# Performance work log

Hardware: AMD Instinct MI355X
Metric: run time of the kernel (lower is better)

## Reference

```python
import jax, jax.numpy as jnp
import numpy as np

B, C, H, W = 4, 64, 64, 64
DQ = 64            # query/key dim (hardcoded 64 in the module)
FP_DIM = 128       # fingerprint_dim
SCALE = 1.0 / 8.0  # 1/sqrt(64)


def setup_inputs() -> dict:
    key = jax.random.key(0)
    ks = jax.random.split(key, 12)
    s = 0.05
    return {
        "x": jax.random.normal(ks[0], (B, C, H, W), jnp.float32),
        "fingerprint": jax.random.normal(ks[1], (B, FP_DIM), jnp.float32),
        # 1x1 conv weights stored as [out_ch, in_ch]
        "Wq": jax.random.normal(ks[2], (DQ, C), jnp.float32) * s,
        "bq": jax.random.normal(ks[3], (DQ,), jnp.float32) * s,
        "Wk": jax.random.normal(ks[4], (DQ, C), jnp.float32) * s,
        "bk": jax.random.normal(ks[5], (DQ,), jnp.float32) * s,
        "Wv": jax.random.normal(ks[6], (C, C), jnp.float32) * s,
        "bv": jax.random.normal(ks[7], (C,), jnp.float32) * s,
        "Wo": jax.random.normal(ks[8], (C, C), jnp.float32) * s,
        "bo": jax.random.normal(ks[9], (C,), jnp.float32) * s,
        "Wfp": jax.random.normal(ks[10], (DQ, FP_DIM), jnp.float32) * s,
        "bfp": jax.random.normal(ks[11], (DQ,), jnp.float32) * s,
    }


def reference(x, fingerprint, Wq, bq, Wk, bk, Wv, bv, Wo, bo, Wfp, bfp):
    b, c, h, w = x.shape
    # fingerprint projection: Linear(fingerprint_dim, 64)
    fp_proj = fingerprint @ Wfp.T + bfp                      # [B, 64]
    # 1x1 convs as channel einsums
    q = jnp.einsum('bchw,oc->bohw', x, Wq) + bq[None, :, None, None]  # [B,64,H,W]
    k = jnp.einsum('bchw,oc->bohw', x, Wk) + bk[None, :, None, None]  # [B,64,H,W]
    v = jnp.einsum('bchw,oc->bohw', x, Wv) + bv[None, :, None, None]  # [B,C,H,W]
    qf = q.reshape(b, DQ, h * w)   # [B,64,N]
    kf = k.reshape(b, DQ, h * w)   # [B,64,N]
    vf = v.reshape(b, c, h * w)    # [B,C,N]
    # attn[b,i,j] = <q_i, k_j>/sqrt(64), softmax over keys j
    attn = jax.nn.softmax(jnp.einsum('bdi,bdj->bij', qf, kf) * SCALE, axis=2)  # [B,N,N]
    out = jnp.einsum('bcj,bij->bci', vf, attn).reshape(b, c, h, w)
    # fingerprint-gated modulation map
    attn_map = jax.nn.sigmoid(jnp.einsum('bdhw,bd->bhw', q, fp_proj))[:, None]  # [B,1,H,W]
    out = out * attn_map + x
    out = jnp.einsum('bchw,oc->bohw', out, Wo) + bo[None, :, None, None]
    return out
```

## Files before the change

### kernel.cpp

```cpp
#include <hip/hip_runtime.h>
#include <cstdint>
#include <cstddef>

#define B_    4
#define C_    64
#define N_    4096
#define FPD_  128
#define QSCALE_ (0.125f * 1.4426950408889634f)

typedef short bf16x8 __attribute__((ext_vector_type(8)));
typedef float f32x4  __attribute__((ext_vector_type(4)));

__device__ inline unsigned short f2bf(float f) {
    union { float f; unsigned int u; } v; v.f = f;
    unsigned int u = v.u;
    return (unsigned short)((u + 0x7FFFu + ((u >> 16) & 1u)) >> 16);
}

__global__ __launch_bounds__(256) void prep_kernel(
    const float* __restrict__ fp, const float* __restrict__ Wfp,
    const float* __restrict__ bfp,
    const float* __restrict__ Wq, const float* __restrict__ bq,
    const float* __restrict__ Wk, const float* __restrict__ bk,
    const float* __restrict__ Wv, const float* __restrict__ bv,
    const float* __restrict__ Wo,
    float* __restrict__ fp_proj, unsigned short* __restrict__ Wb,
    float* __restrict__ bs)
{
    int tid = threadIdx.x;
    if (blockIdx.x == 0) {
        int b = tid >> 6, d = tid & 63;
        float acc = bfp[d];
        for (int i = 0; i < FPD_; ++i)
            acc = fmaf(fp[b * FPD_ + i], Wfp[d * FPD_ + i], acc);
        fp_proj[b * 64 + d] = acc;
        if (tid < 64) {
            bs[tid]       = bq[tid] * QSCALE_;
            bs[64 + tid]  = bk[tid];
            bs[128 + tid] = bv[tid];
        }
    } else {
        int g = (blockIdx.x - 1) * 256 + tid;
        int which = g >> 12, l = g & 4095;
        float v;
        if (which == 0)      v = Wq[l] * QSCALE_;
        else if (which == 1) v = Wk[l];
        else if (which == 2) v = Wv[l];
        else                 v = Wo[l];
        Wb[g] = f2bf(v);
    }
}

__global__ __launch_bounds__(256) void qkv_kernel(
    const float* __restrict__ x, const unsigned short* __restrict__ Wb,
    const float* __restrict__ bs, const float* __restrict__ fp_proj,
    float* __restrict__ gate,
    unsigned short* __restrict__ Qb, unsigned short* __restrict__ Kb,
    unsigned short* __restrict__ Vb)
{
    __shared__ unsigned short xT[64 * 72];
    __shared__ unsigned short rp[64 * 72];

    int tid = threadIdx.x;
    int b  = blockIdx.x >> 6;
    int p0 = (blockIdx.x & 63) << 6;
    const float* xb = x + (size_t)b * (C_ * N_) + p0;

    for (int i = 0; i < 16; ++i) {
        int l = tid + i * 256;
        int c = l >> 6, p = l & 63;
        xT[p * 72 + c] = f2bf(xb[(size_t)c * N_ + p]);
    }
    __syncthreads();

    int lane = tid & 63;
    int wv   = __builtin_amdgcn_readfirstlane(tid >> 6);
    int quad = lane >> 4, l16 = lane & 15;
    int prow = wv * 16 + l16;

    bf16x8 bx0 = *reinterpret_cast<bf16x8*>(&xT[prow * 72 + quad * 8]);
    bf16x8 bx1 = *reinterpret_cast<bf16x8*>(&xT[prow * 72 + 32 + quad * 8]);

    float gp = 0.f;

    for (int pass = 0; pass < 3; ++pass) {
        #pragma unroll
        for (int t4 = 0; t4 < 4; ++t4) {
            int ot = pass * 4 + t4;
            const unsigned short* Wg = Wb + ot * 1024;
            bf16x8 a0 = *reinterpret_cast<const bf16x8*>(&Wg[l16 * 64 + quad * 8]);
            bf16x8 a1 = *reinterpret_cast<const bf16x8*>(&Wg[l16 * 64 + 32 + quad * 8]);
            f32x4 c4 = (f32x4){0.f, 0.f, 0.f, 0.f};
            c4 = __builtin_amdgcn_mfma_f32_16x16x32_bf16(a0, bx0, c4, 0, 0, 0);
            c4 = __builtin_amdgcn_mfma_f32_16x16x32_bf16(a1, bx1, c4, 0, 0, 0);
            float4 bias = *reinterpret_cast<const float4*>(&bs[ot * 16 + quad * 4]);
            c4[0] += bias.x; c4[1] += bias.y; c4[2] += bias.z; c4[3] += bias.w;
            if (pass == 0) {
                float4 fpp = *reinterpret_cast<const float4*>(
                                 &fp_proj[b * 64 + t4 * 16 + quad * 4]);
                gp = fmaf(c4[0], fpp.x, gp); gp = fmaf(c4[1], fpp.y, gp);
                gp = fmaf(c4[2], fpp.z, gp); gp = fmaf(c4[3], fpp.w, gp);
            }
            if (pass < 2) {
                int dd = t4 * 16 + quad * 4;
                ushort2 u01, u23;
                u01.x = f2bf(c4[0]); u01.y = f2bf(c4[1]);
                u23.x = f2bf(c4[2]); u23.y = f2bf(c4[3]);
                *reinterpret_cast<ushort2*>(&rp[prow * 72 + dd])     = u01;
                *reinterpret_cast<ushort2*>(&rp[prow * 72 + dd + 2]) = u23;
            } else {
                #pragma unroll
                for (int j = 0; j < 4; ++j)
                    rp[(t4 * 16 + quad * 4 + j) * 72 + prow] = f2bf(c4[j]);
            }
        }
        if (pass == 0) {
            gp += __shfl_xor(gp, 16);
            gp += __shfl_xor(gp, 32);
            if (l16 == 0 && quad == 0) {  }
            if (lane < 16) {
                int pos = p0 + wv * 16 + lane;
                float s = gp * (1.0f / QSCALE_);
                gate[b * N_ + pos] = 1.f / (1.f + __expf(-s));
            }
        }
        __syncthreads();
        int row = tid >> 2;
        int cb  = (tid & 3) << 4;
        ushort4 u[4];
        #pragma unroll
        for (int k = 0; k < 4; ++k)
            u[k] = *reinterpret_cast<ushort4*>(&rp[row * 72 + cb + k * 4]);
        if (pass == 0) {
            unsigned short* dst = Qb + ((size_t)b * N_ + p0 + row) * 64 + cb;
            #pragma unroll
            for (int k = 0; k < 4; ++k)
                *reinterpret_cast<ushort4*>(dst + k * 4) = u[k];
        } else if (pass == 1) {
            unsigned short* dst = Kb + ((size_t)b * N_ + p0 + row) * 64 + cb;
            #pragma unroll
            for (int k = 0; k < 4; ++k)
                *reinterpret_cast<ushort4*>(dst + k * 4) = u[k];
        } else {
            unsigned short* dst = Vb + ((size_t)b * 64 + row) * N_ + p0 + cb;
            #pragma unroll
            for (int k = 0; k < 4; ++k)
                *reinterpret_cast<ushort4*>(dst + k * 4) = u[k];
        }
        __syncthreads();
    }
}

__global__ __launch_bounds__(256, 4) void attn_kernel(
    const unsigned short* __restrict__ Qb, const unsigned short* __restrict__ Kb,
    const unsigned short* __restrict__ Vb, float* __restrict__ Oattn,
    float* __restrict__ lsum)
{
    __shared__ unsigned short Ks[64 * 72];
    __shared__ unsigned short Vs[64 * 72];
    __shared__ unsigned short Ps[64 * 72];

    int tid = threadIdx.x;
    int bx  = blockIdx.x;
    int qt  = bx >> 4;
    int grp = bx & 15;
    int b   = grp >> 2;
    int ks  = grp & 3;
    int q0  = qt << 6;
    int kbase = ks << 10;

    int lane = tid & 63;
    int wv   = __builtin_amdgcn_readfirstlane(tid >> 6);
    int quad = lane >> 4, l16 = lane & 15;
    int qs0  = wv << 4;

    const unsigned short* Qg = Qb + ((size_t)b * N_ + q0) * 64;
    bf16x8 aq0 = *reinterpret_cast<const bf16x8*>(&Qg[(qs0 + l16) * 64 + quad * 8]);
    bf16x8 aq1 = *reinterpret_cast<const bf16x8*>(&Qg[(qs0 + l16) * 64 + 32 + quad * 8]);

    const unsigned short* Kg = Kb + ((size_t)b * N_ + kbase) * 64;
    const unsigned short* Vg = Vb + (size_t)b * 64 * N_ + kbase;

    int r0 = tid >> 4;
    int cc = (tid & 15) << 2;

    ushort4 kr[4], vr[4];
    #pragma unroll
    for (int i = 0; i < 4; ++i) {
        int r = r0 + 16 * i;
        kr[i] = *reinterpret_cast<const ushort4*>(&Kg[(size_t)r * 64 + cc]);
        vr[i] = *reinterpret_cast<const ushort4*>(&Vg[(size_t)r * N_ + cc]);
    }

    f32x4 oacc[4]; f32x4 lacc = (f32x4){0.f, 0.f, 0.f, 0.f};
    #pragma unroll
    for (int cs = 0; cs < 4; ++cs) oacc[cs] = (f32x4){0.f, 0.f, 0.f, 0.f};
    bf16x8 ones;
    #pragma unroll
    for (int i = 0; i < 8; ++i) ones[i] = (short)0x3F80;

    for (int kt = 0; kt < 16; ++kt) {
        __syncthreads();
        #pragma unroll
        for (int i = 0; i < 4; ++i) {
            int r = r0 + 16 * i;
            *reinterpret_cast<ushort4*>(&Ks[r * 72 + cc]) = kr[i];
            *reinterpret_cast<ushort4*>(&Vs[r * 72 + cc]) = vr[i];
        }
        __syncthreads();
        if (kt < 15) {
            int kk = (kt + 1) << 6;
            #pragma unroll
            for (int i = 0; i < 4; ++i) {
                int r = r0 + 16 * i;
                kr[i] = *reinterpret_cast<const ushort4*>(&Kg[(size_t)(kk + r) * 64 + cc]);
                vr[i] = *reinterpret_cast<const ushort4*>(&Vg[(size_t)r * N_ + kk + cc]);
            }
        }

        #pragma unroll
        for (int kj = 0; kj < 4; ++kj) {
            bf16x8 bk0 = *reinterpret_cast<bf16x8*>(&Ks[(kj * 16 + l16) * 72 + quad * 8]);
            bf16x8 bk1 = *reinterpret_cast<bf16x8*>(&Ks[(kj * 16 + l16) * 72 + 32 + quad * 8]);
            f32x4 s = (f32x4){0.f, 0.f, 0.f, 0.f};
            s = __builtin_amdgcn_mfma_f32_16x16x32_bf16(aq0, bk0, s, 0, 0, 0);
            s = __builtin_amdgcn_mfma_f32_16x16x32_bf16(aq1, bk1, s, 0, 0, 0);
            #pragma unroll
            for (int j = 0; j < 4; ++j) {
                float pv = exp2f(s[j]);
                Ps[(qs0 + quad * 4 + j) * 72 + kj * 16 + l16] = f2bf(pv);
            }
        }
        __asm__ volatile("s_waitcnt lgkmcnt(0)" ::: "memory");

        bf16x8 ap0 = *reinterpret_cast<bf16x8*>(&Ps[(qs0 + l16) * 72 + quad * 8]);
        bf16x8 ap1 = *reinterpret_cast<bf16x8*>(&Ps[(qs0 + l16) * 72 + 32 + quad * 8]);
        lacc = __builtin_amdgcn_mfma_f32_16x16x32_bf16(ap0, ones, lacc, 0, 0, 0);
        lacc = __builtin_amdgcn_mfma_f32_16x16x32_bf16(ap1, ones, lacc, 0, 0, 0);
        #pragma unroll
        for (int cs = 0; cs < 4; ++cs) {
            bf16x8 bv0 = *reinterpret_cast<bf16x8*>(&Vs[(cs * 16 + l16) * 72 + quad * 8]);
            bf16x8 bv1 = *reinterpret_cast<bf16x8*>(&Vs[(cs * 16 + l16) * 72 + 32 + quad * 8]);
            oacc[cs] = __builtin_amdgcn_mfma_f32_16x16x32_bf16(ap0, bv0, oacc[cs], 0, 0, 0);
            oacc[cs] = __builtin_amdgcn_mfma_f32_16x16x32_bf16(ap1, bv1, oacc[cs], 0, 0, 0);
        }
    }

    float* Og = Oattn + ((size_t)b * N_ + q0) * 64;
    #pragma unroll
    for (int j = 0; j < 4; ++j) {
        int row = qs0 + quad * 4 + j;
        #pragma unroll
        for (int cs = 0; cs < 4; ++cs)
            unsafeAtomicAdd(&Og[row * 64 + cs * 16 + l16], oacc[cs][j]);
    }
    if (l16 == 0) {
        #pragma unroll
        for (int j = 0; j < 4; ++j)
            unsafeAtomicAdd(&lsum[b * N_ + q0 + qs0 + quad * 4 + j], lacc[j]);
    }
}

__global__ __launch_bounds__(256) void epi_kernel(
    const float* __restrict__ Oattn, const float* __restrict__ lsum,
    const float* __restrict__ x, const float* __restrict__ gate,
    const unsigned short* __restrict__ Wb, const float* __restrict__ bo,
    float* __restrict__ out)
{
    __shared__ float xs[64 * 68];
    __shared__ float os[64 * 68];

    int tid = threadIdx.x;
    int b  = blockIdx.x >> 6;
    int p0 = (blockIdx.x & 63) << 6;
    const float* xb = x + (size_t)b * (C_ * N_) + p0;

    for (int i = 0; i < 16; ++i) {
        int l = tid + i * 256;
        int c = l >> 6, p = l & 63;
        xs[p * 68 + c] = xb[(size_t)c * N_ + p];
    }
    __syncthreads();

    int lane = tid & 63;
    int wv   = __builtin_amdgcn_readfirstlane(tid >> 6);
    int quad = lane >> 4, l16 = lane & 15;
    int prow = wv * 16 + l16;
    int pos  = p0 + prow;

    float gi = gate[b * N_ + pos] / lsum[b * N_ + pos];
    const float* Og = Oattn + ((size_t)b * N_ + pos) * 64;

    bf16x8 bt0, bt1;
    {
        float4 o0 = *reinterpret_cast<const float4*>(&Og[quad * 8]);
        float4 o1 = *reinterpret_cast<const float4*>(&Og[quad * 8 + 4]);
        float4 xa = *reinterpret_cast<float4*>(&xs[prow * 68 + quad * 8]);
        float4 xc = *reinterpret_cast<float4*>(&xs[prow * 68 + quad * 8 + 4]);
        bt0[0] = f2bf(fmaf(o0.x, gi, xa.x)); bt0[1] = f2bf(fmaf(o0.y, gi, xa.y));
        bt0[2] = f2bf(fmaf(o0.z, gi, xa.z)); bt0[3] = f2bf(fmaf(o0.w, gi, xa.w));
        bt0[4] = f2bf(fmaf(o1.x, gi, xc.x)); bt0[5] = f2bf(fmaf(o1.y, gi, xc.y));
        bt0[6] = f2bf(fmaf(o1.z, gi, xc.z)); bt0[7] = f2bf(fmaf(o1.w, gi, xc.w));
        float4 o2 = *reinterpret_cast<const float4*>(&Og[32 + quad * 8]);
        float4 o3 = *reinterpret_cast<const float4*>(&Og[32 + quad * 8 + 4]);
        float4 xe = *reinterpret_cast<float4*>(&xs[prow * 68 + 32 + quad * 8]);
        float4 xg = *reinterpret_cast<float4*>(&xs[prow * 68 + 32 + quad * 8 + 4]);
        bt1[0] = f2bf(fmaf(o2.x, gi, xe.x)); bt1[1] = f2bf(fmaf(o2.y, gi, xe.y));
        bt1[2] = f2bf(fmaf(o2.z, gi, xe.z)); bt1[3] = f2bf(fmaf(o2.w, gi, xe.w));
        bt1[4] = f2bf(fmaf(o3.x, gi, xg.x)); bt1[5] = f2bf(fmaf(o3.y, gi, xg.y));
        bt1[6] = f2bf(fmaf(o3.z, gi, xg.z)); bt1[7] = f2bf(fmaf(o3.w, gi, xg.w));
    }

    const unsigned short* Wob = Wb + 12288;
    #pragma unroll
    for (int ot = 0; ot < 4; ++ot) {
        bf16x8 a0 = *reinterpret_cast<const bf16x8*>(&Wob[(ot * 16 + l16) * 64 + quad * 8]);
        bf16x8 a1 = *reinterpret_cast<const bf16x8*>(&Wob[(ot * 16 + l16) * 64 + 32 + quad * 8]);
        f32x4 c4 = (f32x4){0.f, 0.f, 0.f, 0.f};
        c4 = __builtin_amdgcn_mfma_f32_16x16x32_bf16(a0, bt0, c4, 0, 0, 0);
        c4 = __builtin_amdgcn_mfma_f32_16x16x32_bf16(a1, bt1, c4, 0, 0, 0);
        float4 bias = *reinterpret_cast<const float4*>(&bo[ot * 16 + quad * 4]);
        c4[0] += bias.x; c4[1] += bias.y; c4[2] += bias.z; c4[3] += bias.w;
        #pragma unroll
        for (int j = 0; j < 4; ++j)
            os[(ot * 16 + quad * 4 + j) * 68 + prow] = c4[j];
    }
    __syncthreads();

    int row = tid >> 2;
    int pb  = (tid & 3) << 4;
    float* ob = out + ((size_t)b * 64 + row) * N_ + p0 + pb;
    #pragma unroll
    for (int k = 0; k < 4; ++k)
        *reinterpret_cast<float4*>(ob + k * 4) =
            *reinterpret_cast<float4*>(&os[row * 68 + pb + k * 4]);
}

extern "C" void kernel_launch(void* const* d_in, const int* in_sizes, int n_in,
                              void* d_out, int out_size, void* d_ws, size_t ws_size,
                              hipStream_t stream)
{
    const float* x   = (const float*)d_in[0];
    const float* fp  = (const float*)d_in[1];
    const float* Wq  = (const float*)d_in[2];
    const float* bq  = (const float*)d_in[3];
    const float* Wk  = (const float*)d_in[4];
    const float* bk  = (const float*)d_in[5];
    const float* Wv  = (const float*)d_in[6];
    const float* bv  = (const float*)d_in[7];
    const float* Wo  = (const float*)d_in[8];
    const float* bo  = (const float*)d_in[9];
    const float* Wfp = (const float*)d_in[10];
    const float* bfp = (const float*)d_in[11];
    float* out = (float*)d_out;

    char* ws = (char*)d_ws;
    float* fp_proj = (float*)(ws);
    float* gate    = (float*)(ws + 1024);
    unsigned short* Qb = (unsigned short*)(ws + 66560);
    unsigned short* Kb = (unsigned short*)(ws + 66560 + 2097152);
    unsigned short* Vb = (unsigned short*)(ws + 66560 + 2 * 2097152);
    float* Oattn = (float*)(ws + 66560 + 3 * 2097152);
    float* lsum  = (float*)(ws + 66560 + 3 * 2097152 + 4194304);
    unsigned short* Wb = (unsigned short*)(ws + 66560 + 3 * 2097152 + 4194304 + 65536);
    float* bs = (float*)(ws + 66560 + 3 * 2097152 + 4194304 + 65536 + 32768);

    hipMemsetAsync(Oattn, 0, 4194304 + 65536, stream);

    hipLaunchKernelGGL(prep_kernel, dim3(65), dim3(256), 0, stream,
                       fp, Wfp, bfp, Wq, bq, Wk, bk, Wv, bv, Wo,
                       fp_proj, Wb, bs);
    hipLaunchKernelGGL(qkv_kernel, dim3(256), dim3(256), 0, stream,
                       x, Wb, bs, fp_proj, gate, Qb, Kb, Vb);
    hipLaunchKernelGGL(attn_kernel, dim3(1024), dim3(256), 0, stream,
                       Qb, Kb, Vb, Oattn, lsum);
    hipLaunchKernelGGL(epi_kernel, dim3(256), dim3(256), 0, stream,
                       Oattn, lsum, x, gate, Wb, bo, out);
}
```

Before: 145.9 us.

## Switch attention to 32x32 MFMA with register P, fuse prep into QKV and epilogue

The attention kernel now uses 32x32x16 bf16 MFMA tiles with K as the A operand. The P matrix is rebuilt in registers through cross-half lane shuffles instead of a shared-memory round trip, and row sums are computed with shuffles rather than a ones-matrix MFMA. The separate prep kernel is removed: each QKV block converts its own weight slice to bf16 and computes the fingerprint projection itself. The QKV and epilogue grids are split across the Q/K/V passes and the output-channel halves for more parallelism. This removes one launch and the LDS traffic for P, at the cost of redundant weight conversion and x loads per block.

```diff
diff --git a/kernel.cpp b/kernel.cpp
--- a/kernel.cpp
+++ b/kernel.cpp
@@ -10,68 +10,87 @@
 
 typedef short bf16x8 __attribute__((ext_vector_type(8)));
 typedef float f32x4  __attribute__((ext_vector_type(4)));
+typedef float f32x16 __attribute__((ext_vector_type(16)));
 
 __device__ inline unsigned short f2bf(float f) {
     union { float f; unsigned int u; } v; v.f = f;
     unsigned int u = v.u;
     return (unsigned short)((u + 0x7FFFu + ((u >> 16) & 1u)) >> 16);
 }
-
-__global__ __launch_bounds__(256) void prep_kernel(
-    const float* __restrict__ fp, const float* __restrict__ Wfp,
-    const float* __restrict__ bfp,
+__device__ inline unsigned int pack2bf(float a, float b) {
+    return (unsigned int)f2bf(a) | ((unsigned int)f2bf(b) << 16);
+}
+
+union frag_u { bf16x8 v; unsigned int u[4]; };
+
+__global__ __launch_bounds__(256) void qkv_kernel(
+    const float* __restrict__ x,
     const float* __restrict__ Wq, const float* __restrict__ bq,
     const float* __restrict__ Wk, const float* __restrict__ bk,
     const float* __restrict__ Wv, const float* __restrict__ bv,
-    const float* __restrict__ Wo,
-    float* __restrict__ fp_proj, unsigned short* __restrict__ Wb,
-    float* __restrict__ bs)
-{
-    int tid = threadIdx.x;
-    if (blockIdx.x == 0) {
-        int b = tid >> 6, d = tid & 63;
-        float acc = bfp[d];
-        for (int i = 0; i < FPD_; ++i)
-            acc = fmaf(fp[b * FPD_ + i], Wfp[d * FPD_ + i], acc);
-        fp_proj[b * 64 + d] = acc;
-        if (tid < 64) {
-            bs[tid]       = bq[tid] * QSCALE_;
-            bs[64 + tid]  = bk[tid];
-            bs[128 + tid] = bv[tid];
-        }
-    } else {
-        int g = (blockIdx.x - 1) * 256 + tid;
-        int which = g >> 12, l = g & 4095;
-        float v;
-        if (which == 0)      v = Wq[l] * QSCALE_;
-        else if (which == 1) v = Wk[l];
-        else if (which == 2) v = Wv[l];
-        else                 v = Wo[l];
-        Wb[g] = f2bf(v);
-    }
-}
-
-__global__ __launch_bounds__(256) void qkv_kernel(
-    const float* __restrict__ x, const unsigned short* __restrict__ Wb,
-    const float* __restrict__ bs, const float* __restrict__ fp_proj,
+    const float* __restrict__ fp, const float* __restrict__ Wfp,
+    const float* __restrict__ bfp,
     float* __restrict__ gate,
     unsigned short* __restrict__ Qb, unsigned short* __restrict__ Kb,
     unsigned short* __restrict__ Vb)
 {
     __shared__ unsigned short xT[64 * 72];
+    __shared__ unsigned short Wl[64 * 72];
     __shared__ unsigned short rp[64 * 72];
-
-    int tid = threadIdx.x;
-    int b  = blockIdx.x >> 6;
-    int p0 = (blockIdx.x & 63) << 6;
+    __shared__ float gredf[256];
+    __shared__ float fpp[64];
+
+    int tid  = threadIdx.x;
+    int bx   = blockIdx.x;
+    int pass = bx >> 8;
+    int rem  = bx & 255;
+    int b  = rem >> 6;
+    int p0 = (rem & 63) << 6;
     const float* xb = x + (size_t)b * (C_ * N_) + p0;
 
+    const float* Wsrc = (pass == 0) ? Wq : (pass == 1) ? Wk : Wv;
+    const float* bsrc = (pass == 0) ? bq : (pass == 1) ? bk : bv;
+    float wscale = (pass == 0) ? QSCALE_ : 1.0f;
+
+    {
+        int o  = tid >> 2;
+        int cb = (tid & 3) << 4;
+        const float4* src = reinterpret_cast<const float4*>(&Wsrc[o * 64 + cb]);
+        float4 w0 = src[0], w1 = src[1], w2 = src[2], w3 = src[3];
+        uint4 lo, hi;
+        lo.x = pack2bf(w0.x * wscale, w0.y * wscale);
+        lo.y = pack2bf(w0.z * wscale, w0.w * wscale);
+        lo.z = pack2bf(w1.x * wscale, w1.y * wscale);
+        lo.w = pack2bf(w1.z * wscale, w1.w * wscale);
+        hi.x = pack2bf(w2.x * wscale, w2.y * wscale);
+        hi.y = pack2bf(w2.z * wscale, w2.w * wscale);
+        hi.z = pack2bf(w3.x * wscale, w3.y * wscale);
+        hi.w = pack2bf(w3.z * wscale, w3.w * wscale);
+        *reinterpret_cast<uint4*>(&Wl[o * 72 + cb])     = lo;
+        *reinterpret_cast<uint4*>(&Wl[o * 72 + cb + 8]) = hi;
+    }
     for (int i = 0; i < 16; ++i) {
         int l = tid + i * 256;
         int c = l >> 6, p = l & 63;
         xT[p * 72 + c] = f2bf(xb[(size_t)c * N_ + p]);
     }
+    if (pass == 0) {
+        int d = tid >> 2, kq = tid & 3;
+        const float4* wrow = reinterpret_cast<const float4*>(&Wfp[d * FPD_ + kq * 32]);
+        const float4* frow = reinterpret_cast<const float4*>(&fp[b * FPD_ + kq * 32]);
+        float s = 0.f;
+        #pragma unroll
+        for (int i = 0; i < 8; ++i) {
+            float4 w4 = wrow[i], f4 = frow[i];
+            s += w4.x * f4.x + w4.y * f4.y + w4.z * f4.z + w4.w * f4.w;
+        }
+        gredf[tid] = s;
+    }
     __syncthreads();
+    if (pass == 0 && tid < 64)
+        fpp[tid] = bfp[tid] + gredf[tid * 4] + gredf[tid * 4 + 1]
+                 + gredf[tid * 4 + 2] + gredf[tid * 4 + 3];
+    if (pass == 0) __syncthreads();
 
     int lane = tid & 63;
     int wv   = __builtin_amdgcn_readfirstlane(tid >> 6);
@@ -82,73 +101,58 @@
     bf16x8 bx1 = *reinterpret_cast<bf16x8*>(&xT[prow * 72 + 32 + quad * 8]);
 
     float gp = 0.f;
-
-    for (int pass = 0; pass < 3; ++pass) {
-        #pragma unroll
-        for (int t4 = 0; t4 < 4; ++t4) {
-            int ot = pass * 4 + t4;
-            const unsigned short* Wg = Wb + ot * 1024;
-            bf16x8 a0 = *reinterpret_cast<const bf16x8*>(&Wg[l16 * 64 + quad * 8]);
-            bf16x8 a1 = *reinterpret_cast<const bf16x8*>(&Wg[l16 * 64 + 32 + quad * 8]);
-            f32x4 c4 = (f32x4){0.f, 0.f, 0.f, 0.f};
-            c4 = __builtin_amdgcn_mfma_f32_16x16x32_bf16(a0, bx0, c4, 0, 0, 0);
-            c4 = __builtin_amdgcn_mfma_f32_16x16x32_bf16(a1, bx1, c4, 0, 0, 0);
-            float4 bias = *reinterpret_cast<const float4*>(&bs[ot * 16 + quad * 4]);
-            c4[0] += bias.x; c4[1] += bias.y; c4[2] += bias.z; c4[3] += bias.w;
-            if (pass == 0) {
-                float4 fpp = *reinterpret_cast<const float4*>(
-                                 &fp_proj[b * 64 + t4 * 16 + quad * 4]);
-                gp = fmaf(c4[0], fpp.x, gp); gp = fmaf(c4[1], fpp.y, gp);
-                gp = fmaf(c4[2], fpp.z, gp); gp = fmaf(c4[3], fpp.w, gp);
-            }
-            if (pass < 2) {
-                int dd = t4 * 16 + quad * 4;
-                ushort2 u01, u23;
-                u01.x = f2bf(c4[0]); u01.y = f2bf(c4[1]);
-                u23.x = f2bf(c4[2]); u23.y = f2bf(c4[3]);
-                *reinterpret_cast<ushort2*>(&rp[prow * 72 + dd])     = u01;
-                *reinterpret_cast<ushort2*>(&rp[prow * 72 + dd + 2]) = u23;
-            } else {
-                #pragma unroll
-                for (int j = 0; j < 4; ++j)
-                    rp[(t4 * 16 + quad * 4 + j) * 72 + prow] = f2bf(c4[j]);
-            }
-        }
+    #pragma unroll
+    for (int t4 = 0; t4 < 4; ++t4) {
+        bf16x8 a0 = *reinterpret_cast<bf16x8*>(&Wl[(t4 * 16 + l16) * 72 + quad * 8]);
+        bf16x8 a1 = *reinterpret_cast<bf16x8*>(&Wl[(t4 * 16 + l16) * 72 + 32 + quad * 8]);
+        f32x4 c4 = (f32x4){0.f, 0.f, 0.f, 0.f};
+        c4 = __builtin_amdgcn_mfma_f32_16x16x32_bf16(a0, bx0, c4, 0, 0, 0);
+        c4 = __builtin_amdgcn_mfma_f32_16x16x32_bf16(a1, bx1, c4, 0, 0, 0);
+        float4 bias = *reinterpret_cast<const float4*>(&bsrc[t4 * 16 + quad * 4]);
+        c4[0] += bias.x * wscale; c4[1] += bias.y * wscale;
+        c4[2] += bias.z * wscale; c4[3] += bias.w * wscale;
         if (pass == 0) {
-            gp += __shfl_xor(gp, 16);
-            gp += __shfl_xor(gp, 32);
-            if (l16 == 0 && quad == 0) {  }
-            if (lane < 16) {
-                int pos = p0 + wv * 16 + lane;
-                float s = gp * (1.0f / QSCALE_);
-                gate[b * N_ + pos] = 1.f / (1.f + __expf(-s));
-            }
-        }
-        __syncthreads();
-        int row = tid >> 2;
-        int cb  = (tid & 3) << 4;
-        ushort4 u[4];
-        #pragma unroll
-        for (int k = 0; k < 4; ++k)
-            u[k] = *reinterpret_cast<ushort4*>(&rp[row * 72 + cb + k * 4]);
-        if (pass == 0) {
-            unsigned short* dst = Qb + ((size_t)b * N_ + p0 + row) * 64 + cb;
+            gp = fmaf(c4[0], fpp[t4 * 16 + quad * 4 + 0], gp);
+            gp = fmaf(c4[1], fpp[t4 * 16 + quad * 4 + 1], gp);
+            gp = fmaf(c4[2], fpp[t4 * 16 + quad * 4 + 2], gp);
+            gp = fmaf(c4[3], fpp[t4 * 16 + quad * 4 + 3], gp);
+        }
+        if (pass < 2) {
+            int dd = t4 * 16 + quad * 4;
+            *reinterpret_cast<ushort2*>(&rp[prow * 72 + dd]) =
+                (ushort2){f2bf(c4[0]), f2bf(c4[1])};
+            *reinterpret_cast<ushort2*>(&rp[prow * 72 + dd + 2]) =
+                (ushort2){f2bf(c4[2]), f2bf(c4[3])};
+        } else {
             #pragma unroll
-            for (int k = 0; k < 4; ++k)
-                *reinterpret_cast<ushort4*>(dst + k * 4) = u[k];
-        } else if (pass == 1) {
-            unsigned short* dst = Kb + ((size_t)b * N_ + p0 + row) * 64 + cb;
-            #pragma unroll
-            for (int k = 0; k < 4; ++k)
-                *reinterpret_cast<ushort4*>(dst + k * 4) = u[k];
-        } else {
-            unsigned short* dst = Vb + ((size_t)b * 64 + row) * N_ + p0 + cb;
-            #pragma unroll
-            for (int k = 0; k < 4; ++k)
-                *reinterpret_cast<ushort4*>(dst + k * 4) = u[k];
-        }
-        __syncthreads();
-    }
+            for (int j = 0; j < 4; ++j)
+                rp[(t4 * 16 + quad * 4 + j) * 72 + prow] = f2bf(c4[j]);
+        }
+    }
+    if (pass == 0) {
+        gp += __shfl_xor(gp, 16);
+        gp += __shfl_xor(gp, 32);
+        if (lane < 16) {
+            int pos = p0 + wv * 16 + lane;
+            float s = gp * (1.0f / QSCALE_);
+            gate[b * N_ + pos] = 1.f / (1.f + __expf(-s));
+        }
+    }
+    __syncthreads();
+
+    int row = tid >> 2;
+    int cb  = (tid & 3) << 4;
+    ushort4 u[4];
+    #pragma unroll
+    for (int k = 0; k < 4; ++k)
+        u[k] = *reinterpret_cast<ushort4*>(&rp[row * 72 + cb + k * 4]);
+    unsigned short* dst;
+    if (pass == 0)      dst = Qb + ((size_t)b * N_ + p0 + row) * 64 + cb;
+    else if (pass == 1) dst = Kb + ((size_t)b * N_ + p0 + row) * 64 + cb;
+    else                dst = Vb + ((size_t)b * 64 + row) * N_ + p0 + cb;
+    #pragma unroll
+    for (int k = 0; k < 4; ++k)
+        *reinterpret_cast<ushort4*>(dst + k * 4) = u[k];
 }
 
 __global__ __launch_bounds__(256, 4) void attn_kernel(
@@ -158,7 +162,6 @@
 {
     __shared__ unsigned short Ks[64 * 72];
     __shared__ unsigned short Vs[64 * 72];
-    __shared__ unsigned short Ps[64 * 72];
 
     int tid = threadIdx.x;
     int bx  = blockIdx.x;
@@ -171,114 +174,153 @@
 
     int lane = tid & 63;
     int wv   = __builtin_amdgcn_readfirstlane(tid >> 6);
-    int quad = lane >> 4, l16 = lane & 15;
-    int qs0  = wv << 4;
-
-    const unsigned short* Qg = Qb + ((size_t)b * N_ + q0) * 64;
-    bf16x8 aq0 = *reinterpret_cast<const bf16x8*>(&Qg[(qs0 + l16) * 64 + quad * 8]);
-    bf16x8 aq1 = *reinterpret_cast<const bf16x8*>(&Qg[(qs0 + l16) * 64 + 32 + quad * 8]);
+    int qh   = wv & 1;
+    int kh   = wv >> 1;
+    int h    = lane >> 5;
+    int m    = lane & 31;
+
+    const unsigned short* Qg =
+        Qb + ((size_t)b * N_ + q0 + qh * 32 + m) * 64 + h * 8;
+    bf16x8 bq[4];
+    #pragma unroll
+    for (int c = 0; c < 4; ++c)
+        bq[c] = *reinterpret_cast<const bf16x8*>(Qg + c * 16);
 
     const unsigned short* Kg = Kb + ((size_t)b * N_ + kbase) * 64;
     const unsigned short* Vg = Vb + (size_t)b * 64 * N_ + kbase;
 
-    int r0 = tid >> 4;
-    int cc = (tid & 15) << 2;
-
-    ushort4 kr[4], vr[4];
-    #pragma unroll
-    for (int i = 0; i < 4; ++i) {
-        int r = r0 + 16 * i;
-        kr[i] = *reinterpret_cast<const ushort4*>(&Kg[(size_t)r * 64 + cc]);
-        vr[i] = *reinterpret_cast<const ushort4*>(&Vg[(size_t)r * N_ + cc]);
-    }
-
-    f32x4 oacc[4]; f32x4 lacc = (f32x4){0.f, 0.f, 0.f, 0.f};
-    #pragma unroll
-    for (int cs = 0; cs < 4; ++cs) oacc[cs] = (f32x4){0.f, 0.f, 0.f, 0.f};
-    bf16x8 ones;
-    #pragma unroll
-    for (int i = 0; i < 8; ++i) ones[i] = (short)0x3F80;
+    int srow = tid >> 3;
+    int scol = (tid & 7) << 3;
+
+    uint4 kr[2], vr[2];
+    #pragma unroll
+    for (int i = 0; i < 2; ++i) {
+        int r = srow + 32 * i;
+        kr[i] = *reinterpret_cast<const uint4*>(&Kg[(size_t)r * 64 + scol]);
+        vr[i] = *reinterpret_cast<const uint4*>(&Vg[(size_t)r * N_ + scol]);
+    }
+
+    f32x16 oacc[2];
+    #pragma unroll
+    for (int ct = 0; ct < 2; ++ct)
+        #pragma unroll
+        for (int r = 0; r < 16; ++r) oacc[ct][r] = 0.f;
+    float lacc = 0.f;
+
+    const unsigned short* KsA = &Ks[(kh * 32 + m) * 72 + h * 8];
+    const unsigned short* Vs0 = &Vs[m * 72 + kh * 32 + h * 8];
 
     for (int kt = 0; kt < 16; ++kt) {
         __syncthreads();
         #pragma unroll
-        for (int i = 0; i < 4; ++i) {
-            int r = r0 + 16 * i;
-            *reinterpret_cast<ushort4*>(&Ks[r * 72 + cc]) = kr[i];
-            *reinterpret_cast<ushort4*>(&Vs[r * 72 + cc]) = vr[i];
+        for (int i = 0; i < 2; ++i) {
+            int r = srow + 32 * i;
+            *reinterpret_cast<uint4*>(&Ks[r * 72 + scol]) = kr[i];
+            *reinterpret_cast<uint4*>(&Vs[r * 72 + scol]) = vr[i];
         }
         __syncthreads();
         if (kt < 15) {
             int kk = (kt + 1) << 6;
             #pragma unroll
-            for (int i = 0; i < 4; ++i) {
-                int r = r0 + 16 * i;
-                kr[i] = *reinterpret_cast<const ushort4*>(&Kg[(size_t)(kk + r) * 64 + cc]);
-                vr[i] = *reinterpret_cast<const ushort4*>(&Vg[(size_t)r * N_ + kk + cc]);
+            for (int i = 0; i < 2; ++i) {
+                int r = srow + 32 * i;
+                kr[i] = *reinterpret_cast<const uint4*>(&Kg[(size_t)(kk + r) * 64 + scol]);
+                vr[i] = *reinterpret_cast<const uint4*>(&Vg[(size_t)r * N_ + kk + scol]);
             }
         }
 
-        #pragma unroll
-        for (int kj = 0; kj < 4; ++kj) {
-            bf16x8 bk0 = *reinterpret_cast<bf16x8*>(&Ks[(kj * 16 + l16) * 72 + quad * 8]);
-            bf16x8 bk1 = *reinterpret_cast<bf16x8*>(&Ks[(kj * 16 + l16) * 72 + 32 + quad * 8]);
-            f32x4 s = (f32x4){0.f, 0.f, 0.f, 0.f};
-            s = __builtin_amdgcn_mfma_f32_16x16x32_bf16(aq0, bk0, s, 0, 0, 0);
-            s = __builtin_amdgcn_mfma_f32_16x16x32_bf16(aq1, bk1, s, 0, 0, 0);
-            #pragma unroll
-            for (int j = 0; j < 4; ++j) {
-                float pv = exp2f(s[j]);
-                Ps[(qs0 + quad * 4 + j) * 72 + kj * 16 + l16] = f2bf(pv);
-            }
-        }
-        __asm__ volatile("s_waitcnt lgkmcnt(0)" ::: "memory");
-
-        bf16x8 ap0 = *reinterpret_cast<bf16x8*>(&Ps[(qs0 + l16) * 72 + quad * 8]);
-        bf16x8 ap1 = *reinterpret_cast<bf16x8*>(&Ps[(qs0 + l16) * 72 + 32 + quad * 8]);
-        lacc = __builtin_amdgcn_mfma_f32_16x16x32_bf16(ap0, ones, lacc, 0, 0, 0);
-        lacc = __builtin_amdgcn_mfma_f32_16x16x32_bf16(ap1, ones, lacc, 0, 0, 0);
-        #pragma unroll
-        for (int cs = 0; cs < 4; ++cs) {
-            bf16x8 bv0 = *reinterpret_cast<bf16x8*>(&Vs[(cs * 16 + l16) * 72 + quad * 8]);
-            bf16x8 bv1 = *reinterpret_cast<bf16x8*>(&Vs[(cs * 16 + l16) * 72 + 32 + quad * 8]);
-            oacc[cs] = __builtin_amdgcn_mfma_f32_16x16x32_bf16(ap0, bv0, oacc[cs], 0, 0, 0);
-            oacc[cs] = __builtin_amdgcn_mfma_f32_16x16x32_bf16(ap1, bv1, oacc[cs], 0, 0, 0);
-        }
-    }
-
-    float* Og = Oattn + ((size_t)b * N_ + q0) * 64;
-    #pragma unroll
-    for (int j = 0; j < 4; ++j) {
-        int row = qs0 + quad * 4 + j;
-        #pragma unroll
-        for (int cs = 0; cs < 4; ++cs)
-            unsafeAtomicAdd(&Og[row * 64 + cs * 16 + l16], oacc[cs][j]);
-    }
-    if (l16 == 0) {
-        #pragma unroll
-        for (int j = 0; j < 4; ++j)
-            unsafeAtomicAdd(&lsum[b * N_ + q0 + qs0 + quad * 4 + j], lacc[j]);
-    }
+        f32x16 s;
+        #pragma unroll
+        for (int r = 0; r < 16; ++r) s[r] = 0.f;
+        #pragma unroll
+        for (int c = 0; c < 4; ++c) {
+            bf16x8 ak = *reinterpret_cast<const bf16x8*>(KsA + c * 16);
+            s = __builtin_amdgcn_mfma_f32_32x32x16_bf16(ak, bq[c], s, 0, 0, 0);
+        }
+
+        float p[16]; float rsum = 0.f;
+        #pragma unroll
+        for (int r = 0; r < 16; ++r) { p[r] = exp2f(s[r]); rsum += p[r]; }
+        lacc += rsum + __shfl_xor(rsum, 32);
+        unsigned int pk[8];
+        #pragma unroll
+        for (int i = 0; i < 8; ++i) pk[i] = pack2bf(p[2 * i], p[2 * i + 1]);
+
+        frag_u ap0, ap1;
+        {
+            unsigned int s0 = h ? pk[0] : pk[2];
+            unsigned int s1 = h ? pk[1] : pk[3];
+            unsigned int r0 = __shfl_xor(s0, 32);
+            unsigned int r1 = __shfl_xor(s1, 32);
+            ap0.u[0] = h ? r0 : pk[0];
+            ap0.u[1] = h ? r1 : pk[1];
+            ap0.u[2] = h ? pk[2] : r0;
+            ap0.u[3] = h ? pk[3] : r1;
+            unsigned int s2 = h ? pk[4] : pk[6];
+            unsigned int s3 = h ? pk[5] : pk[7];
+            unsigned int r2 = __shfl_xor(s2, 32);
+            unsigned int r3 = __shfl_xor(s3, 32);
+            ap1.u[0] = h ? r2 : pk[4];
+            ap1.u[1] = h ? r3 : pk[5];
+            ap1.u[2] = h ? pk[6] : r2;
+            ap1.u[3] = h ? pk[7] : r3;
+        }
+
+        #pragma unroll
+        for (int ct = 0; ct < 2; ++ct) {
+            bf16x8 bv0 = *reinterpret_cast<const bf16x8*>(Vs0 + ct * 32 * 72);
+            bf16x8 bv1 = *reinterpret_cast<const bf16x8*>(Vs0 + ct * 32 * 72 + 16);
+            oacc[ct] = __builtin_amdgcn_mfma_f32_32x32x16_bf16(ap0.v, bv0, oacc[ct], 0, 0, 0);
+            oacc[ct] = __builtin_amdgcn_mfma_f32_32x32x16_bf16(ap1.v, bv1, oacc[ct], 0, 0, 0);
+        }
+    }
+
+    float* Og = Oattn + ((size_t)b * N_ + q0 + qh * 32) * 64;
+    #pragma unroll
+    for (int ct = 0; ct < 2; ++ct)
+        #pragma unroll
+        for (int r = 0; r < 16; ++r) {
+            int ql = (r & 3) + 8 * (r >> 2) + 4 * h;
+            unsafeAtomicAdd(&Og[ql * 64 + ct * 32 + m], oacc[ct][r]);
+        }
+    if (h == 0)
+        unsafeAtomicAdd(&lsum[b * N_ + q0 + qh * 32 + m], lacc);
 }
 
 __global__ __launch_bounds__(256) void epi_kernel(
     const float* __restrict__ Oattn, const float* __restrict__ lsum,
     const float* __restrict__ x, const float* __restrict__ gate,
-    const unsigned short* __restrict__ Wb, const float* __restrict__ bo,
+    const float* __restrict__ Wo, const float* __restrict__ bo,
     float* __restrict__ out)
 {
     __shared__ float xs[64 * 68];
-    __shared__ float os[64 * 68];
-
-    int tid = threadIdx.x;
-    int b  = blockIdx.x >> 6;
-    int p0 = (blockIdx.x & 63) << 6;
+    __shared__ unsigned short Wl[32 * 72];
+    __shared__ float os[32 * 68];
+
+    int tid  = threadIdx.x;
+    int bx   = blockIdx.x;
+    int half = bx >> 8;
+    int rem  = bx & 255;
+    int b  = rem >> 6;
+    int p0 = (rem & 63) << 6;
     const float* xb = x + (size_t)b * (C_ * N_) + p0;
 
     for (int i = 0; i < 16; ++i) {
         int l = tid + i * 256;
         int c = l >> 6, p = l & 63;
         xs[p * 68 + c] = xb[(size_t)c * N_ + p];
+    }
+    {
+        int ol = tid >> 3;
+        int cb = (tid & 7) << 3;
+        const float4* src = reinterpret_cast<const float4*>(
+            &Wo[(half * 32 + ol) * 64 + cb]);
+        float4 w0 = src[0], w1 = src[1];
+        uint2 pkd;
+        pkd.x = pack2bf(w0.x, w0.y); pkd.y = pack2bf(w0.z, w0.w);
+        *reinterpret_cast<uint2*>(&Wl[ol * 72 + cb]) = pkd;
+        pkd.x = pack2bf(w1.x, w1.y); pkd.y = pack2bf(w1.z, w1.w);
+        *reinterpret_cast<uint2*>(&Wl[ol * 72 + cb + 4]) = pkd;
     }
     __syncthreads();
 
@@ -311,11 +353,11 @@
         bt1[6] = f2bf(fmaf(o3.z, gi, xg.z)); bt1[7] = f2bf(fmaf(o3.w, gi, xg.w));
     }
 
-    const unsigned short* Wob = Wb + 12288;
-    #pragma unroll
-    for (int ot = 0; ot < 4; ++ot) {
-        bf16x8 a0 = *reinterpret_cast<const bf16x8*>(&Wob[(ot * 16 + l16) * 64 + quad * 8]);
-        bf16x8 a1 = *reinterpret_cast<const bf16x8*>(&Wob[(ot * 16 + l16) * 64 + 32 + quad * 8]);
+    #pragma unroll
+    for (int tt = 0; tt < 2; ++tt) {
+        int ot = half * 2 + tt;
+        bf16x8 a0 = *reinterpret_cast<bf16x8*>(&Wl[(tt * 16 + l16) * 72 + quad * 8]);
+        bf16x8 a1 = *reinterpret_cast<bf16x8*>(&Wl[(tt * 16 + l16) * 72 + 32 + quad * 8]);
         f32x4 c4 = (f32x4){0.f, 0.f, 0.f, 0.f};
         c4 = __builtin_amdgcn_mfma_f32_16x16x32_bf16(a0, bt0, c4, 0, 0, 0);
         c4 = __builtin_amdgcn_mfma_f32_16x16x32_bf16(a1, bt1, c4, 0, 0, 0);
@@ -323,17 +365,15 @@
         c4[0] += bias.x; c4[1] += bias.y; c4[2] += bias.z; c4[3] += bias.w;
         #pragma unroll
         for (int j = 0; j < 4; ++j)
-            os[(ot * 16 + quad * 4 + j) * 68 + prow] = c4[j];
+            os[(tt * 16 + quad * 4 + j) * 68 + prow] = c4[j];
     }
     __syncthreads();
 
-    int row = tid >> 2;
-    int pb  = (tid & 3) << 4;
-    float* ob = out + ((size_t)b * 64 + row) * N_ + p0 + pb;
-    #pragma unroll
-    for (int k = 0; k < 4; ++k)
-        *reinterpret_cast<float4*>(ob + k * 4) =
-            *reinterpret_cast<float4*>(&os[row * 68 + pb + k * 4]);
+    int row = tid >> 3;
+    int pb  = (tid & 7) << 3;
+    float* ob = out + ((size_t)b * 64 + half * 32 + row) * N_ + p0 + pb;
+    *reinterpret_cast<float4*>(ob)     = *reinterpret_cast<float4*>(&os[row * 68 + pb]);
+    *reinterpret_cast<float4*>(ob + 4) = *reinterpret_cast<float4*>(&os[row * 68 + pb + 4]);
 }
 
 extern "C" void kernel_launch(void* const* d_in, const int* in_sizes, int n_in,
@@ -355,25 +395,20 @@
     float* out = (float*)d_out;
 
     char* ws = (char*)d_ws;
-    float* fp_proj = (float*)(ws);
-    float* gate    = (float*)(ws + 1024);
-    unsigned short* Qb = (unsigned short*)(ws + 66560);
-    unsigned short* Kb = (unsigned short*)(ws + 66560 + 2097152);
-    unsigned short* Vb = (unsigned short*)(ws + 66560 + 2 * 2097152);
-    float* Oattn = (float*)(ws + 66560 + 3 * 2097152);
-    float* lsum  = (float*)(ws + 66560 + 3 * 2097152 + 4194304);
-    unsigned short* Wb = (unsigned short*)(ws + 66560 + 3 * 2097152 + 4194304 + 65536);
-    float* bs = (float*)(ws + 66560 + 3 * 2097152 + 4194304 + 65536 + 32768);
+    float* gate = (float*)(ws);
+    unsigned short* Qb = (unsigned short*)(ws + 65536);
+    unsigned short* Kb = (unsigned short*)(ws + 65536 + 2097152);
+    unsigned short* Vb = (unsigned short*)(ws + 65536 + 2 * 2097152);
+    float* Oattn = (float*)(ws + 65536 + 3 * 2097152);
+    float* lsum  = (float*)(ws + 65536 + 3 * 2097152 + 4194304);
 
     hipMemsetAsync(Oattn, 0, 4194304 + 65536, stream);
 
-    hipLaunchKernelGGL(prep_kernel, dim3(65), dim3(256), 0, stream,
-                       fp, Wfp, bfp, Wq, bq, Wk, bk, Wv, bv, Wo,
-                       fp_proj, Wb, bs);
-    hipLaunchKernelGGL(qkv_kernel, dim3(256), dim3(256), 0, stream,
-                       x, Wb, bs, fp_proj, gate, Qb, Kb, Vb);
+    hipLaunchKernelGGL(qkv_kernel, dim3(768), dim3(256), 0, stream,
+                       x, Wq, bq, Wk, bk, Wv, bv, fp, Wfp, bfp,
+                       gate, Qb, Kb, Vb);
     hipLaunchKernelGGL(attn_kernel, dim3(1024), dim3(256), 0, stream,
                        Qb, Kb, Vb, Oattn, lsum);
-    hipLaunchKernelGGL(epi_kernel, dim3(256), dim3(256), 0, stream,
-                       Oattn, lsum, x, gate, Wb, bo, out);
-}
+    hipLaunchKernelGGL(epi_kernel, dim3(512), dim3(256), 0, stream,
+                       Oattn, lsum, x, gate, Wo, bo, out);
+}
```

Result: slower. 177.7 us (+21.8%).
